# Performance work log

Measured on AMD Instinct MI355X. Metric: run time of the kernel, lower is better.

## Reference

```python
import jax, jax.numpy as jnp
import numpy as np

DIM = 4096
N_HEADS = 32
N_KV_HEADS = 8
HEAD_DIM = 128
EPS = 1e-6
B, S = 1, 2048


def setup_inputs() -> dict:
    key = jax.random.key(0)
    ks = jax.random.split(key, 8)
    x = jax.random.normal(ks[0], (B, S, DIM), dtype=jnp.float32)
    # Standard RoPE cos/sin table, broadcast to (B, S, HEAD_DIM)
    inv_freq = 1.0 / (10000.0 ** (np.arange(0, HEAD_DIM, 2, dtype=np.float32) / HEAD_DIM))
    t = np.arange(S, dtype=np.float32)
    freqs = np.outer(t, inv_freq)  # (S, HEAD_DIM/2)
    emb = np.concatenate([freqs, freqs], axis=-1)  # (S, HEAD_DIM)
    cos = jnp.broadcast_to(jnp.cos(emb)[None], (B, S, HEAD_DIM))
    sin = jnp.broadcast_to(jnp.sin(emb)[None], (B, S, HEAD_DIM))
    std = 0.02
    wq = jax.random.normal(ks[1], (N_HEADS * HEAD_DIM, DIM), dtype=jnp.float32) * std
    wk = jax.random.normal(ks[2], (N_KV_HEADS * HEAD_DIM, DIM), dtype=jnp.float32) * std
    wv = jax.random.normal(ks[3], (N_KV_HEADS * HEAD_DIM, DIM), dtype=jnp.float32) * std
    wo = jax.random.normal(ks[4], (DIM, N_HEADS * HEAD_DIM), dtype=jnp.float32) * std
    q_norm_w = jnp.ones((HEAD_DIM,), dtype=jnp.float32) + 0.1 * jax.random.normal(ks[5], (HEAD_DIM,), dtype=jnp.float32)
    k_norm_w = jnp.ones((HEAD_DIM,), dtype=jnp.float32) + 0.1 * jax.random.normal(ks[6], (HEAD_DIM,), dtype=jnp.float32)
    return {"x": x, "cos": cos, "sin": sin, "wq": wq, "wk": wk, "wv": wv,
            "wo": wo, "q_norm_w": q_norm_w, "k_norm_w": k_norm_w}


def _rmsnorm(x, w):
    var = jnp.mean(jnp.square(x), axis=-1, keepdims=True)
    return x * jax.lax.rsqrt(var + EPS) * w


def _rotate_half(x):
    h = x.shape[-1] // 2
    return jnp.concatenate([-x[..., h:], x[..., :h]], axis=-1)


def reference(x, cos, sin, wq, wk, wv, wo, q_norm_w, k_norm_w):
    bs, seqlen, _ = x.shape
    # QKV projections (Linear with weight of shape (out, in), no bias)
    xq = (x @ wq.T).reshape(bs, seqlen, N_HEADS, HEAD_DIM)
    xk = (x @ wk.T).reshape(bs, seqlen, N_KV_HEADS, HEAD_DIM)
    xv = (x @ wv.T).reshape(bs, seqlen, N_KV_HEADS, HEAD_DIM)
    # QK RMSNorm (after projection, before RoPE)
    xq = _rmsnorm(xq, q_norm_w)
    xk = _rmsnorm(xk, k_norm_w)
    # RoPE: cos/sin (B, S, D) -> broadcast over head axis
    c = cos[:, :, None, :]
    s = sin[:, :, None, :]
    xq = xq * c + _rotate_half(xq) * s
    xk = xk * c + _rotate_half(xk) * s
    # GQA: repeat kv heads
    n_rep = N_HEADS // N_KV_HEADS
    xk = jnp.repeat(xk, n_rep, axis=2)
    xv = jnp.repeat(xv, n_rep, axis=2)
    # (B, H, S, D)
    q = xq.transpose(0, 2, 1, 3)
    k = xk.transpose(0, 2, 1, 3)
    v = xv.transpose(0, 2, 1, 3)
    scale = HEAD_DIM ** -0.5
    scores = jnp.einsum('bhqd,bhkd->bhqk', q, k) * scale
    causal = jnp.tril(jnp.ones((seqlen, seqlen), dtype=bool))
    scores = jnp.where(causal, scores, jnp.finfo(scores.dtype).min)
    probs = jax.nn.softmax(scores, axis=-1)
    out = jnp.einsum('bhqk,bhkd->bhqd', probs, v)
    out = out.transpose(0, 2, 1, 3).reshape(bs, seqlen, N_HEADS * HEAD_DIM)
    return out @ wo.T
```

## Files before the change

### kernel.cpp

```cpp
#include <hip/hip_runtime.h>


#define S_LEN 2048
#define DIM 4096
#define NH 32
#define NKV 8
#define HD 128
#define SCALE 0.08838834764831845f

typedef __attribute__((ext_vector_type(8))) short short8;
typedef __attribute__((ext_vector_type(4))) float f32x4;

__device__ __forceinline__ float bf2f(unsigned short u) {
  union { unsigned i; float f; } c; c.i = ((unsigned)u) << 16; return c.f;
}
__device__ __forceinline__ unsigned short f2bf(float f) {
  union { float f; unsigned u; } c; c.f = f;
  return (unsigned short)((c.u + 0x7fffu + ((c.u >> 16) & 1u)) >> 16);
}
__device__ __forceinline__ void cvt8(const float* __restrict__ g,
                                     unsigned short* __restrict__ d) {
  const float4 a = *(const float4*)g;
  const float4 b = *(const float4*)(g + 4);
  short8 p;
  p[0] = (short)f2bf(a.x); p[1] = (short)f2bf(a.y);
  p[2] = (short)f2bf(a.z); p[3] = (short)f2bf(a.w);
  p[4] = (short)f2bf(b.x); p[5] = (short)f2bf(b.y);
  p[6] = (short)f2bf(b.z); p[7] = (short)f2bf(b.w);
  *(short8*)d = p;
}
__device__ __forceinline__ void storeC(float* p, float v) { *p = v; }
__device__ __forceinline__ void storeC(unsigned short* p, float v) { *p = f2bf(v); }

#define G_X   1048576u
#define G_WQ  2097152u
#define G_WK   524288u
#define G_WV   524288u
#define G_QKV (G_WQ + G_WK + G_WV)

__global__ __launch_bounds__(256)
void cvt_all(const float* __restrict__ x,  const float* __restrict__ wq,
             const float* __restrict__ wk, const float* __restrict__ wv,
             const float* __restrict__ wo,
             unsigned short* __restrict__ xb,
             unsigned short* __restrict__ wqkvb,
             unsigned short* __restrict__ wob) {
  const size_t g = (size_t)blockIdx.x * 256 + threadIdx.x;
  if (g < G_X) {
    cvt8(x + g * 8, xb + g * 8);
  } else if (g < G_X + G_QKV) {
    const size_t o = g - G_X;
    const float* s = (o < G_WQ) ? wq + o * 8
                   : (o < G_WQ + G_WK) ? wk + (o - G_WQ) * 8
                                       : wv + (o - G_WQ - G_WK) * 8;
    cvt8(s, wqkvb + o * 8);
  } else {
    const size_t o = g - (G_X + G_QKV);
    cvt8(wo + o * 8, wob + o * 8);
  }
}

template <int QKV, typename TC>
__global__ __launch_bounds__(256)
void gemm16(const unsigned short* __restrict__ A,
            const unsigned short* __restrict__ B,
            TC* __restrict__ C0,
            unsigned short* __restrict__ Ck,
            unsigned short* __restrict__ Cv, int K) {
  __shared__ unsigned short lsA[128 * 64];
  __shared__ unsigned short lsB[128 * 64];

  const int t    = threadIdx.x;
  const int lane = t & 63;
  const int w    = t >> 6;
  const int m0   = blockIdx.y * 128;
  const int n0   = blockIdx.x * 128;

  f32x4 acc[4][4];
#pragma unroll
  for (int a = 0; a < 4; ++a)
#pragma unroll
    for (int b = 0; b < 4; ++b)
#pragma unroll
      for (int e = 0; e < 4; ++e) acc[a][b][e] = 0.f;

  const int l15  = lane & 15;
  const int qd   = lane >> 4;
  const int wr   = w >> 1, wc = w & 1;
  const int sr8  = lane >> 3;
  const int skg  = (lane & 7) ^ sr8;
  const int l7   = l15 & 7;

  const int nkb = K >> 6;
  for (int kb = 0; kb < nkb; ++kb) {
    const int k0 = kb << 6;
#pragma unroll
    for (int c = 0; c < 4; ++c) {
      const int chunk = c * 4 + w;
      const int row   = chunk * 8 + sr8;
      const unsigned short* ga = A + (size_t)(m0 + row) * K + k0 + skg * 8;
      const unsigned short* gb = B + (size_t)(n0 + row) * K + k0 + skg * 8;
      __builtin_amdgcn_global_load_lds(
          (const __attribute__((address_space(1))) void*)ga,
          (__attribute__((address_space(3))) void*)(lsA + chunk * 512), 16, 0, 0);
      __builtin_amdgcn_global_load_lds(
          (const __attribute__((address_space(1))) void*)gb,
          (__attribute__((address_space(3))) void*)(lsB + chunk * 512), 16, 0, 0);
    }
    asm volatile("s_waitcnt vmcnt(0)" ::: "memory");
    __syncthreads();

#pragma unroll
    for (int half = 0; half < 2; ++half) {
      const int kg = (half * 4 + qd) ^ l7;
      short8 af[4], bf[4];
#pragma unroll
      for (int mi = 0; mi < 4; ++mi)
        af[mi] = *(const short8*)(lsA + (wr * 64 + mi * 16 + l15) * 64 + kg * 8);
#pragma unroll
      for (int ni = 0; ni < 4; ++ni)
        bf[ni] = *(const short8*)(lsB + (wc * 64 + ni * 16 + l15) * 64 + kg * 8);
#pragma unroll
      for (int mi = 0; mi < 4; ++mi)
#pragma unroll
        for (int ni = 0; ni < 4; ++ni)
          acc[mi][ni] = __builtin_amdgcn_mfma_f32_16x16x32_bf16(
              af[mi], bf[ni], acc[mi][ni], 0, 0, 0);
    }
    __syncthreads();
  }

#pragma unroll
  for (int mi = 0; mi < 4; ++mi)
#pragma unroll
    for (int i = 0; i < 4; ++i) {
      const int grow = m0 + wr * 64 + mi * 16 + qd * 4 + i;
#pragma unroll
      for (int ni = 0; ni < 4; ++ni) {
        const int gcol = n0 + wc * 64 + ni * 16 + l15;
        if (QKV) {
          if (n0 < 4096)
            storeC((unsigned short*)C0 + (size_t)grow * 4096 + gcol,
                   acc[mi][ni][i]);
          else if (n0 < 5120)
            Ck[(size_t)grow * 1024 + (gcol - 4096)] = f2bf(acc[mi][ni][i]);
          else
            Cv[(size_t)(gcol - 5120) * S_LEN + grow] = f2bf(acc[mi][ni][i]);
        } else {
          storeC(C0 + (size_t)grow * 4096 + gcol, acc[mi][ni][i]);
        }
      }
    }
}

__global__ __launch_bounds__(512)
void norm_rope(unsigned short* __restrict__ qb, unsigned short* __restrict__ kb,
               const float* __restrict__ cosb, const float* __restrict__ sinb,
               const float* __restrict__ qw, const float* __restrict__ kw) {
  const int s    = blockIdx.x;
  const int w    = threadIdx.x >> 6;
  const int l    = threadIdx.x & 63;
  const int hh   = blockIdx.y * 8 + w;

  unsigned short* p; const float* wt;
  if (hh < NH) { p = qb + (size_t)s * (NH * HD) + hh * HD; wt = qw; }
  else         { p = kb + (size_t)s * (NKV * HD) + (hh - NH) * HD; wt = kw; }

  const float v0 = bf2f(p[l]);
  const float v1 = bf2f(p[l + 64]);
  float ss = v0 * v0 + v1 * v1;
#pragma unroll
  for (int off = 32; off; off >>= 1) ss += __shfl_xor(ss, off);
  const float r = rsqrtf(ss * (1.f / 128.f) + 1e-6f);

  const float xn0 = v0 * r * wt[l];
  const float xn1 = v1 * r * wt[l + 64];
  const float c0 = cosb[s * HD + l],      s0 = sinb[s * HD + l];
  const float c1 = cosb[s * HD + l + 64], s1 = sinb[s * HD + l + 64];
  float o0 = xn0 * c0 - xn1 * s0;
  float o1 = xn1 * c1 + xn0 * s1;
  if (hh < NH) { o0 *= SCALE; o1 *= SCALE; }
  p[l]      = f2bf(o0);
  p[l + 64] = f2bf(o1);
}

#define PSTR 72

#define STAGE_KV(KT, BUF)                                                      \
  {                                                                            \
    unsigned short* ksb = ks + (BUF) * 8192;                                   \
    unsigned short* vtb = vt + (BUF) * 8192;                                   \
    _Pragma("unroll")                                                          \
    for (int c = 0; c < 4; ++c) {                                              \
      const int chunk = w * 4 + c;                                             \
      const int key = chunk * 4 + kr16;                                        \
      const int dg  = (lane & 15) ^ (key & 15);                                \
      const unsigned short* gk = kB + (size_t)((KT) * 64 + key) * (NKV * HD) + \
                                 kvh * HD + dg * 8;                            \
      __builtin_amdgcn_global_load_lds(                                        \
          (const __attribute__((address_space(1))) void*)gk,                   \
          (__attribute__((address_space(3))) void*)(ksb + chunk * 512),        \
          16, 0, 0);                                                           \
      const int dv = chunk * 8 + vr8;                                          \
      const unsigned short* gv = vT + (size_t)(kvh * HD + dv) * S_LEN +        \
                                 (KT) * 64 + vkg * 8;                          \
      __builtin_amdgcn_global_load_lds(                                        \
          (const __attribute__((address_space(1))) void*)gv,                   \
          (__attribute__((address_space(3))) void*)(vtb + chunk * 512),        \
          16, 0, 0);                                                           \
    }                                                                          \
  }

__global__ __launch_bounds__(256)
void attn_mfma(const unsigned short* __restrict__ qB,
               const unsigned short* __restrict__ kB,
               const unsigned short* __restrict__ vT,
               unsigned short* __restrict__ oB) {
  __shared__ unsigned short ks[2 * 64 * 128];
  __shared__ unsigned short vt[2 * 64 * 128];
  __shared__ unsigned short Ps[4 * 16 * PSTR];

  const int t    = threadIdx.x;
  const int lane = t & 63;
  const int w    = t >> 6;
  const int h    = blockIdx.y;
  const int qt   = (h & 16) ? (15 - blockIdx.x) : blockIdx.x;
  const int q0   = qt * 128;
  const int kvh  = h >> 2;
  const int l15  = lane & 15;
  const int qd   = lane >> 4;
  const int l7   = l15 & 7;

  const int kr16 = lane >> 4;
  const int vr8  = lane >> 3;
  const int vkg  = (lane & 7) ^ (vr8 & 7);

  short8 qf[2][4];
#pragma unroll
  for (int f = 0; f < 2; ++f) {
    const unsigned short* qp =
        qB + (size_t)(q0 + w * 32 + f * 16 + l15) * (NH * HD) + h * HD + qd * 8;
#pragma unroll
    for (int s = 0; s < 4; ++s) qf[f][s] = *(const short8*)(qp + s * 32);
  }

  f32x4 O[2][8];
#pragma unroll
  for (int f = 0; f < 2; ++f)
#pragma unroll
    for (int nt = 0; nt < 8; ++nt)
#pragma unroll
      for (int e = 0; e < 4; ++e) O[f][nt][e] = 0.f;
  float l_i[2][4] = {{0.f, 0.f, 0.f, 0.f}, {0.f, 0.f, 0.f, 0.f}};

  unsigned short* Pw = Ps + w * (16 * PSTR);

  const int nkt = 2 * qt + 2;

  STAGE_KV(0, 0);

  for (int kt = 0; kt < nkt; ++kt) {
    const int cur = kt & 1;
    const int kn  = (kt + 1 < nkt) ? (kt + 1) : kt;
    STAGE_KV(kn, cur ^ 1);
    asm volatile("s_waitcnt vmcnt(8)" ::: "memory");
    __builtin_amdgcn_s_barrier();

    const unsigned short* ksb = ks + cur * 8192;
    const unsigned short* vtb = vt + cur * 8192;

    const int dk = kt - 2 * qt;
    const bool active = (dk <= 0) || (w >= 2);
    if (active) {
      f32x4 S[2][4];
      __builtin_amdgcn_s_setprio(1);
#pragma unroll
      for (int ct = 0; ct < 4; ++ct) {
#pragma unroll
        for (int e = 0; e < 4; ++e) { S[0][ct][e] = 0.f; S[1][ct][e] = 0.f; }
#pragma unroll
        for (int s = 0; s < 4; ++s) {
          const int kg = (s * 4 + qd) ^ l15;
          const short8 kf =
              *(const short8*)(ksb + (ct * 16 + l15) * 128 + kg * 8);
          S[0][ct] = __builtin_amdgcn_mfma_f32_16x16x32_bf16(qf[0][s], kf,
                                                             S[0][ct], 0, 0, 0);
          S[1][ct] = __builtin_amdgcn_mfma_f32_16x16x32_bf16(qf[1][s], kf,
                                                             S[1][ct], 0, 0, 0);
        }
      }
      __builtin_amdgcn_s_setprio(0);

      if (dk >= 0) {
#pragma unroll
        for (int f = 0; f < 2; ++f)
#pragma unroll
          for (int ct = 0; ct < 4; ++ct)
#pragma unroll
            for (int i = 0; i < 4; ++i) {
              const int krel = dk * 64 + ct * 16 + l15;
              const int rrel = w * 32 + f * 16 + qd * 4 + i;
              if (krel > rrel) S[f][ct][i] = -1e30f;
            }
      }

      short8 pf[2][2];
#pragma unroll
      for (int f = 0; f < 2; ++f) {
#pragma unroll
        for (int ct = 0; ct < 4; ++ct)
#pragma unroll
          for (int i = 0; i < 4; ++i) {
            const float e = __expf(S[f][ct][i]);
            l_i[f][i] += e;
            Pw[(qd * 4 + i) * PSTR + ct * 16 + l15] = f2bf(e);
          }
        pf[f][0] = *(const short8*)(Pw + l15 * PSTR + qd * 8);
        pf[f][1] = *(const short8*)(Pw + l15 * PSTR + 32 + qd * 8);
      }

      {
        const int kg0 = qd ^ l7;
        const int kg1 = (4 + qd) ^ l7;
        __builtin_amdgcn_s_setprio(1);
#pragma unroll
        for (int nt = 0; nt < 8; ++nt) {
          const short8 vf0 =
              *(const short8*)(vtb + (nt * 16 + l15) * 64 + kg0 * 8);
          const short8 vf1 =
              *(const short8*)(vtb + (nt * 16 + l15) * 64 + kg1 * 8);
          O[0][nt] = __builtin_amdgcn_mfma_f32_16x16x32_bf16(pf[0][0], vf0,
                                                             O[0][nt], 0, 0, 0);
          O[1][nt] = __builtin_amdgcn_mfma_f32_16x16x32_bf16(pf[1][0], vf0,
                                                             O[1][nt], 0, 0, 0);
          O[0][nt] = __builtin_amdgcn_mfma_f32_16x16x32_bf16(pf[0][1], vf1,
                                                             O[0][nt], 0, 0, 0);
          O[1][nt] = __builtin_amdgcn_mfma_f32_16x16x32_bf16(pf[1][1], vf1,
                                                             O[1][nt], 0, 0, 0);
        }
        __builtin_amdgcn_s_setprio(0);
      }
    }
    __builtin_amdgcn_s_barrier();
    __builtin_amdgcn_sched_barrier(0);
  }

  float linv[2][4];
#pragma unroll
  for (int f = 0; f < 2; ++f)
#pragma unroll
    for (int i = 0; i < 4; ++i) {
      float s = l_i[f][i];
#pragma unroll
      for (int off = 1; off < 16; off <<= 1) s += __shfl_xor(s, off);
      linv[f][i] = 1.f / s;
    }
#pragma unroll
  for (int f = 0; f < 2; ++f)
#pragma unroll
    for (int nt = 0; nt < 8; ++nt)
#pragma unroll
      for (int i = 0; i < 4; ++i) {
        const size_t row = (size_t)(q0 + w * 32 + f * 16 + qd * 4 + i);
        oB[row * (NH * HD) + h * HD + nt * 16 + l15] =
            f2bf(O[f][nt][i] * linv[f][i]);
      }
}

extern "C" void kernel_launch(void* const* d_in, const int* in_sizes, int n_in,
                              void* d_out, int out_size, void* d_ws, size_t ws_size,
                              hipStream_t stream) {
  const float* x    = (const float*)d_in[0];
  const float* cosb = (const float*)d_in[1];
  const float* sinb = (const float*)d_in[2];
  const float* wq   = (const float*)d_in[3];
  const float* wk   = (const float*)d_in[4];
  const float* wv   = (const float*)d_in[5];
  const float* wo   = (const float*)d_in[6];
  const float* qnw  = (const float*)d_in[7];
  const float* knw  = (const float*)d_in[8];

  unsigned short* q     = (unsigned short*)d_ws;
  unsigned short* k     = q + (size_t)S_LEN * DIM;
  unsigned short* vT    = k + (size_t)S_LEN * NKV * HD;
  unsigned short* att   = vT + (size_t)NKV * HD * S_LEN;
  unsigned short* xb    = att + (size_t)S_LEN * DIM;
  unsigned short* wqkvb = xb + (size_t)S_LEN * DIM;
  unsigned short* wob   = wqkvb + (size_t)6144 * DIM;

  cvt_all<<<dim3(24576), dim3(256), 0, stream>>>(x, wq, wk, wv, wo, xb, wqkvb,
                                                 wob);
  gemm16<1, unsigned short>
      <<<dim3(48, 16), dim3(256), 0, stream>>>(xb, wqkvb, q, k, vT, DIM);
  norm_rope<<<dim3(S_LEN, 5), dim3(512), 0, stream>>>(q, k, cosb, sinb,
                                                      qnw, knw);
  attn_mfma<<<dim3(S_LEN / 128, NH), dim3(256), 0, stream>>>(q, k, vT, att);
  gemm16<0, float>
      <<<dim3(32, 16), dim3(256), 0, stream>>>(att, wob, (float*)d_out,
                                               nullptr, nullptr, DIM);
}
```

Before: 529.5 us.

## Use 128x256 tile, 512-thread GEMM for output projection

Replaces the output-projection GEMM launch with a new kernel that uses 128x256 output tiles, 8 waves per block, double-buffered direct global-to-LDS loads with an XOR swizzle, and raised wave priority around the MFMA section. The wider tile halves the number of blocks (256 instead of 512) and increases reuse of each A tile across more output columns. The cost is fewer blocks to fill the GPU's compute units and a larger LDS footprint per block, which may reduce occupancy.

```diff
diff --git a/kernel.cpp b/kernel.cpp
--- a/kernel.cpp
+++ b/kernel.cpp
@@ -151,6 +151,109 @@
         }
       }
     }
+}
+
+#define WTILE (128 * 64 + 256 * 64)
+
+__global__ __launch_bounds__(512)
+void gemm_wide(const unsigned short* __restrict__ A,
+               const unsigned short* __restrict__ B,
+               float* __restrict__ C0) {
+  __shared__ unsigned short ls[2 * WTILE];
+
+  const int t    = threadIdx.x;
+  const int lane = t & 63;
+  const int w    = t >> 6;
+  const int wr   = w >> 2;
+  const int wc   = w & 3;
+  const int m0   = blockIdx.y * 128;
+  const int n0   = blockIdx.x * 256;
+  const int l15  = lane & 15;
+  const int qd   = lane >> 4;
+  const int l7   = l15 & 7;
+  const int sr8  = lane >> 3;
+  const int skg  = (lane & 7) ^ sr8;
+
+  f32x4 acc[4][4];
+#pragma unroll
+  for (int a = 0; a < 4; ++a)
+#pragma unroll
+    for (int b = 0; b < 4; ++b)
+#pragma unroll
+      for (int e = 0; e < 4; ++e) acc[a][b][e] = 0.f;
+
+#define STAGE_W(KT, BUF)                                                       \
+  {                                                                            \
+    unsigned short* la = ls + (BUF) * WTILE;                                   \
+    unsigned short* lb = la + 8192;                                            \
+    const int k0s = (KT) << 6;                                                 \
+    _Pragma("unroll")                                                          \
+    for (int j = 0; j < 2; ++j) {                                              \
+      const int ca  = w * 2 + j;                   \
+      const unsigned short* ga =                                               \
+          A + (size_t)(m0 + ca * 8 + sr8) * DIM + k0s + skg * 8;               \
+      __builtin_amdgcn_global_load_lds(                                        \
+          (const __attribute__((address_space(1))) void*)ga,                   \
+          (__attribute__((address_space(3))) void*)(la + ca * 512), 16, 0, 0); \
+    }                                                                          \
+    _Pragma("unroll")                                                          \
+    for (int j = 0; j < 4; ++j) {                                              \
+      const int cb  = w * 4 + j;                   \
+      const unsigned short* gb =                                               \
+          B + (size_t)(n0 + cb * 8 + sr8) * DIM + k0s + skg * 8;               \
+      __builtin_amdgcn_global_load_lds(                                        \
+          (const __attribute__((address_space(1))) void*)gb,                   \
+          (__attribute__((address_space(3))) void*)(lb + cb * 512), 16, 0, 0); \
+    }                                                                          \
+  }
+
+  STAGE_W(0, 0);
+
+  const int nkb = DIM >> 6;
+  for (int kb = 0; kb < nkb; ++kb) {
+    const int cur = kb & 1;
+    const int kn  = (kb + 1 < nkb) ? (kb + 1) : kb;
+    STAGE_W(kn, cur ^ 1);
+    asm volatile("s_waitcnt vmcnt(6)" ::: "memory");
+    __builtin_amdgcn_s_barrier();
+
+    const unsigned short* la = ls + cur * WTILE;
+    const unsigned short* lb = la + 8192;
+
+    __builtin_amdgcn_s_setprio(1);
+#pragma unroll
+    for (int half = 0; half < 2; ++half) {
+      const int kg = (half * 4 + qd) ^ l7;
+      short8 af[4], bf[4];
+#pragma unroll
+      for (int mi = 0; mi < 4; ++mi)
+        af[mi] = *(const short8*)(la + (wr * 64 + mi * 16 + l15) * 64 + kg * 8);
+#pragma unroll
+      for (int ni = 0; ni < 4; ++ni)
+        bf[ni] = *(const short8*)(lb + (wc * 64 + ni * 16 + l15) * 64 + kg * 8);
+#pragma unroll
+      for (int mi = 0; mi < 4; ++mi)
+#pragma unroll
+        for (int ni = 0; ni < 4; ++ni)
+          acc[mi][ni] = __builtin_amdgcn_mfma_f32_16x16x32_bf16(
+              af[mi], bf[ni], acc[mi][ni], 0, 0, 0);
+    }
+    __builtin_amdgcn_s_setprio(0);
+    __builtin_amdgcn_s_barrier();
+  }
+
+#pragma unroll
+  for (int mi = 0; mi < 4; ++mi)
+#pragma unroll
+    for (int i = 0; i < 4; ++i) {
+      const int grow = m0 + wr * 64 + mi * 16 + qd * 4 + i;
+#pragma unroll
+      for (int ni = 0; ni < 4; ++ni) {
+        const int gcol = n0 + wc * 64 + ni * 16 + l15;
+        C0[(size_t)grow * 4096 + gcol] = acc[mi][ni][i];
+      }
+    }
+#undef STAGE_W
 }
 
 __global__ __launch_bounds__(512)
@@ -395,7 +498,5 @@
   norm_rope<<<dim3(S_LEN, 5), dim3(512), 0, stream>>>(q, k, cosb, sinb,
                                                       qnw, knw);
   attn_mfma<<<dim3(S_LEN / 128, NH), dim3(256), 0, stream>>>(q, k, vT, att);
-  gemm16<0, float>
-      <<<dim3(32, 16), dim3(256), 0, stream>>>(att, wob, (float*)d_out,
-                                               nullptr, nullptr, DIM);
-}
+  gemm_wide<<<dim3(16, 16), dim3(512), 0, stream>>>(att, wob, (float*)d_out);
+}
```

Result: no change. 526.5 us (-0.6%).

## Double-buffer GEMM LDS staging and vectorize norm_rope with 16-lane groups

Applied to the files above, without the earlier changes.

The GEMM kernel now double-buffers its A/B tiles in LDS. It issues global-to-LDS loads for the next K block before computing the current one, waits with a partial vmcnt, and raises wave priority around the MFMA section, so load latency overlaps compute. The norm/RoPE kernel is rewritten so each 16-lane group handles one head with 8-element vector loads and stores, and the rotate-half partner comes from a lane shuffle. This doubles LDS use per GEMM block, which may lower occupancy, and correctness relies on the vmcnt(8) count matching the outstanding loads.

```diff
diff --git a/kernel.cpp b/kernel.cpp
--- a/kernel.cpp
+++ b/kernel.cpp
@@ -60,6 +60,28 @@
   }
 }
 
+#define STAGE_G(KT, BUF)                                                       \
+  {                                                                            \
+    const int k0s = (KT) << 6;                                                 \
+    unsigned short* la = lsA + (BUF) * 8192;                                   \
+    unsigned short* lb = lsB + (BUF) * 8192;                                   \
+    _Pragma("unroll")                                                          \
+    for (int c = 0; c < 4; ++c) {                                              \
+      const int chunk = c * 4 + w;                           \
+      const int row   = chunk * 8 + sr8;                                       \
+      const unsigned short* ga = A + (size_t)(m0 + row) * K + k0s + skg * 8;   \
+      const unsigned short* gb = B + (size_t)(n0 + row) * K + k0s + skg * 8;   \
+      __builtin_amdgcn_global_load_lds(                                        \
+          (const __attribute__((address_space(1))) void*)ga,                   \
+          (__attribute__((address_space(3))) void*)(la + chunk * 512),         \
+          16, 0, 0);                                                           \
+      __builtin_amdgcn_global_load_lds(                                        \
+          (const __attribute__((address_space(1))) void*)gb,                   \
+          (__attribute__((address_space(3))) void*)(lb + chunk * 512),         \
+          16, 0, 0);                                                           \
+    }                                                                          \
+  }
+
 template <int QKV, typename TC>
 __global__ __launch_bounds__(256)
 void gemm16(const unsigned short* __restrict__ A,
@@ -67,8 +89,8 @@
             TC* __restrict__ C0,
             unsigned short* __restrict__ Ck,
             unsigned short* __restrict__ Cv, int K) {
-  __shared__ unsigned short lsA[128 * 64];
-  __shared__ unsigned short lsB[128 * 64];
+  __shared__ unsigned short lsA[2 * 128 * 64];
+  __shared__ unsigned short lsB[2 * 128 * 64];
 
   const int t    = threadIdx.x;
   const int lane = t & 63;
@@ -92,34 +114,30 @@
   const int l7   = l15 & 7;
 
   const int nkb = K >> 6;
+
+  STAGE_G(0, 0);
+
   for (int kb = 0; kb < nkb; ++kb) {
-    const int k0 = kb << 6;
-#pragma unroll
-    for (int c = 0; c < 4; ++c) {
-      const int chunk = c * 4 + w;
-      const int row   = chunk * 8 + sr8;
-      const unsigned short* ga = A + (size_t)(m0 + row) * K + k0 + skg * 8;
-      const unsigned short* gb = B + (size_t)(n0 + row) * K + k0 + skg * 8;
-      __builtin_amdgcn_global_load_lds(
-          (const __attribute__((address_space(1))) void*)ga,
-          (__attribute__((address_space(3))) void*)(lsA + chunk * 512), 16, 0, 0);
-      __builtin_amdgcn_global_load_lds(
-          (const __attribute__((address_space(1))) void*)gb,
-          (__attribute__((address_space(3))) void*)(lsB + chunk * 512), 16, 0, 0);
-    }
-    asm volatile("s_waitcnt vmcnt(0)" ::: "memory");
-    __syncthreads();
-
+    const int cur = kb & 1;
+    const int kn  = (kb + 1 < nkb) ? (kb + 1) : kb;
+    STAGE_G(kn, cur ^ 1);
+    asm volatile("s_waitcnt vmcnt(8)" ::: "memory");
+    __builtin_amdgcn_s_barrier();
+
+    const unsigned short* la = lsA + cur * 8192;
+    const unsigned short* lb = lsB + cur * 8192;
+
+    __builtin_amdgcn_s_setprio(1);
 #pragma unroll
     for (int half = 0; half < 2; ++half) {
       const int kg = (half * 4 + qd) ^ l7;
       short8 af[4], bf[4];
 #pragma unroll
       for (int mi = 0; mi < 4; ++mi)
-        af[mi] = *(const short8*)(lsA + (wr * 64 + mi * 16 + l15) * 64 + kg * 8);
+        af[mi] = *(const short8*)(la + (wr * 64 + mi * 16 + l15) * 64 + kg * 8);
 #pragma unroll
       for (int ni = 0; ni < 4; ++ni)
-        bf[ni] = *(const short8*)(lsB + (wc * 64 + ni * 16 + l15) * 64 + kg * 8);
+        bf[ni] = *(const short8*)(lb + (wc * 64 + ni * 16 + l15) * 64 + kg * 8);
 #pragma unroll
       for (int mi = 0; mi < 4; ++mi)
 #pragma unroll
@@ -127,7 +145,8 @@
           acc[mi][ni] = __builtin_amdgcn_mfma_f32_16x16x32_bf16(
               af[mi], bf[ni], acc[mi][ni], 0, 0, 0);
     }
-    __syncthreads();
+    __builtin_amdgcn_s_setprio(0);
+    __builtin_amdgcn_s_barrier();
   }
 
 #pragma unroll
@@ -153,35 +172,55 @@
     }
 }
 
-__global__ __launch_bounds__(512)
+__global__ __launch_bounds__(256)
 void norm_rope(unsigned short* __restrict__ qb, unsigned short* __restrict__ kb,
                const float* __restrict__ cosb, const float* __restrict__ sinb,
                const float* __restrict__ qw, const float* __restrict__ kw) {
-  const int s    = blockIdx.x;
-  const int w    = threadIdx.x >> 6;
-  const int l    = threadIdx.x & 63;
-  const int hh   = blockIdx.y * 8 + w;
-
-  unsigned short* p; const float* wt;
-  if (hh < NH) { p = qb + (size_t)s * (NH * HD) + hh * HD; wt = qw; }
-  else         { p = kb + (size_t)s * (NKV * HD) + (hh - NH) * HD; wt = kw; }
-
-  const float v0 = bf2f(p[l]);
-  const float v1 = bf2f(p[l + 64]);
-  float ss = v0 * v0 + v1 * v1;
-#pragma unroll
-  for (int off = 32; off; off >>= 1) ss += __shfl_xor(ss, off);
+  const int t    = threadIdx.x;
+  const int g    = t & 15;
+  const int inst = blockIdx.x * 16 + (t >> 4);
+
+  unsigned short* p; const float* wt; int s; bool isq;
+  if (inst < S_LEN * NH) {
+    s = inst >> 5;
+    p = qb + (size_t)s * (NH * HD) + (inst & 31) * HD;
+    wt = qw; isq = true;
+  } else {
+    const int i2 = inst - S_LEN * NH;
+    s = i2 >> 3;
+    p = kb + (size_t)s * (NKV * HD) + (i2 & 7) * HD;
+    wt = kw; isq = false;
+  }
+  const int d0 = g * 8;
+
+  const short8 v = *(const short8*)(p + d0);
+  float x[8];
+  float ss = 0.f;
+#pragma unroll
+  for (int j = 0; j < 8; ++j) {
+    x[j] = bf2f((unsigned short)v[j]);
+    ss += x[j] * x[j];
+  }
+#pragma unroll
+  for (int off = 1; off < 16; off <<= 1) ss += __shfl_xor(ss, off);
   const float r = rsqrtf(ss * (1.f / 128.f) + 1e-6f);
 
-  const float xn0 = v0 * r * wt[l];
-  const float xn1 = v1 * r * wt[l + 64];
-  const float c0 = cosb[s * HD + l],      s0 = sinb[s * HD + l];
-  const float c1 = cosb[s * HD + l + 64], s1 = sinb[s * HD + l + 64];
-  float o0 = xn0 * c0 - xn1 * s0;
-  float o1 = xn1 * c1 + xn0 * s1;
-  if (hh < NH) { o0 *= SCALE; o1 *= SCALE; }
-  p[l]      = f2bf(o0);
-  p[l + 64] = f2bf(o1);
+  float xn[8];
+#pragma unroll
+  for (int j = 0; j < 8; ++j) xn[j] = x[j] * r * wt[d0 + j];
+
+  const float sgn = (g < 8) ? -1.f : 1.f;
+  const float* cp = cosb + s * HD + d0;
+  const float* sp = sinb + s * HD + d0;
+  short8 o;
+#pragma unroll
+  for (int j = 0; j < 8; ++j) {
+    const float pr = __shfl_xor(xn[j], 8);
+    float ov = xn[j] * cp[j] + sgn * pr * sp[j];
+    if (isq) ov *= SCALE;
+    o[j] = (short)f2bf(ov);
+  }
+  *(short8*)(p + d0) = o;
 }
 
 #define PSTR 72
@@ -392,8 +431,8 @@
                                                  wob);
   gemm16<1, unsigned short>
       <<<dim3(48, 16), dim3(256), 0, stream>>>(xb, wqkvb, q, k, vT, DIM);
-  norm_rope<<<dim3(S_LEN, 5), dim3(512), 0, stream>>>(q, k, cosb, sinb,
-                                                      qnw, knw);
+  norm_rope<<<dim3((S_LEN * (NH + NKV)) / 16), dim3(256), 0, stream>>>(
+      q, k, cosb, sinb, qnw, knw);
   attn_mfma<<<dim3(S_LEN / 128, NH), dim3(256), 0, stream>>>(q, k, vT, att);
   gemm16<0, float>
       <<<dim3(32, 16), dim3(256), 0, stream>>>(att, wob, (float*)d_out,
```

New measurement: 552.7 us. +4.4%, slower.
